# Performance work log

Hardware: AMD Instinct MI355X
Metric: run time of the kernel (lower is better)

The kernel has to match this reference:

```python
import jax, jax.numpy as jnp
import numpy as np

B, S, D, H = 4, 2048, 1024, 16
HD = D // H


def setup_inputs() -> dict:
    key = jax.random.key(0)
    ks = jax.random.split(key, 5)
    scale = 0.02
    return {
        "x": jax.random.normal(ks[0], (B, S, D), dtype=jnp.float32),
        "Wq": jax.random.normal(ks[1], (D, D), dtype=jnp.float32) * scale,
        "Wk": jax.random.normal(ks[2], (D, D), dtype=jnp.float32) * scale,
        "Wv": jax.random.normal(ks[3], (D, D), dtype=jnp.float32) * scale,
        "Wo": jax.random.normal(ks[4], (D, D), dtype=jnp.float32) * scale,
    }


def reference(x, Wq, Wk, Wv, Wo):
    b, s, d = x.shape
    # Linear layers (torch Linear: y = x @ W.T), no bias
    q = jnp.einsum('bsd,ed->bse', x, Wq).reshape(b, s, H, HD).transpose(0, 2, 1, 3)
    k = jnp.einsum('bsd,ed->bse', x, Wk).reshape(b, s, H, HD).transpose(0, 2, 1, 3)
    v = jnp.einsum('bsd,ed->bse', x, Wv).reshape(b, s, H, HD).transpose(0, 2, 1, 3)
    # [B,H,S,S] attention scores
    scores = jnp.einsum('bhqd,bhkd->bhqk', q, k)
    causal = jnp.tril(jnp.ones((s, s), dtype=bool))
    scores = jnp.where(causal, scores, -jnp.inf)
    # faithful to source: mask first, then scale, then softmax
    weights = jax.nn.softmax(scores / jnp.sqrt(jnp.float32(HD)), axis=-1)
    # dropout p=0.0 (eval): identity
    ctx = jnp.einsum('bhqk,bhkd->bhqd', weights, v)
    ctx = ctx.transpose(0, 2, 1, 3).reshape(b, s, d)
    return jnp.einsum('bsd,ed->bse', ctx, Wo)
```

## Files before the change

kernel.cpp:

```cpp
#include <hip/hip_runtime.h>
#include <math.h>

typedef unsigned short u16;
typedef __attribute__((ext_vector_type(8))) short short8;
typedef __attribute__((ext_vector_type(4))) float f32x4;
typedef __attribute__((ext_vector_type(16))) float f32x16;
typedef __attribute__((ext_vector_type(4))) unsigned int u32x4;

constexpr int Bb = 4, S_LEN = 2048, DMODEL = 1024, NH = 16;
constexpr int MTOT = Bb * S_LEN;

#define QSCALE 0.18033688011112042f

__device__ __forceinline__ u16 f2bf(float f) {
    union { float f; unsigned u; } v; v.f = f;
    unsigned r = v.u + 0x7FFFu + ((v.u >> 16) & 1u);
    return (u16)(r >> 16);
}

__device__ __forceinline__ float exp2_fast(float x) {
#if __has_builtin(__builtin_amdgcn_exp2f)
    return __builtin_amdgcn_exp2f(x);
#else
    float r; asm("v_exp_f32 %0, %1" : "=v"(r) : "v"(x)); return r;
#endif
}

__device__ __forceinline__ unsigned pk_bf16(float s0, float s1) {
    unsigned pk;
    asm("v_cvt_pk_bf16_f32 %0, %1, %2" : "=v"(pk) : "v"(s0), "v"(s1));
    return pk;
}

__device__ __forceinline__ void load_lds16(const void* g, void* l) {
    __builtin_amdgcn_global_load_lds(
        (const __attribute__((address_space(1))) unsigned int*)g,
        (__attribute__((address_space(3))) unsigned int*)l, 16, 0, 0);
}

__global__ __launch_bounds__(256)
void cvt_all(const float* __restrict__ x,
             const float* __restrict__ w0, const float* __restrict__ w1,
             const float* __restrict__ w2, const float* __restrict__ w3,
             u16* __restrict__ xb, u16* __restrict__ b0, u16* __restrict__ b1,
             u16* __restrict__ b2, u16* __restrict__ b3)
{
    int gid = blockIdx.x * 256 + threadIdx.x;
    constexpr int NXo = (MTOT * DMODEL) / 8;
    constexpr int NWo = (DMODEL * DMODEL) / 8;
    const float* s; u16* d; int o;
    float sc = 1.0f;
    if (gid < NXo) { s = x; d = xb; o = gid; }
    else {
        int t = gid - NXo;
        int w = t >> 17;
        o = t & (NWo - 1);
        s = (w == 0) ? w0 : (w == 1) ? w1 : (w == 2) ? w2 : w3;
        d = (w == 0) ? b0 : (w == 1) ? b1 : (w == 2) ? b2 : b3;
        if (w == 0) sc = QSCALE;
    }
    const float4* sp = (const float4*)(s + (size_t)o * 8);
    float4 a = sp[0], bq = sp[1];
    short8 ov;
    ov[0] = (short)f2bf(a.x * sc);  ov[1] = (short)f2bf(a.y * sc);
    ov[2] = (short)f2bf(a.z * sc);  ov[3] = (short)f2bf(a.w * sc);
    ov[4] = (short)f2bf(bq.x * sc); ov[5] = (short)f2bf(bq.y * sc);
    ov[6] = (short)f2bf(bq.z * sc); ov[7] = (short)f2bf(bq.w * sc);
    *(short8*)(d + (size_t)o * 8) = ov;
}

__global__ __launch_bounds__(256, 2)
void gemm_qkv(const u16* __restrict__ X,
              const u16* __restrict__ W0, const u16* __restrict__ W1, const u16* __restrict__ W2,
              u16* __restrict__ Qo, u16* __restrict__ Ko, u16* __restrict__ VT,
              int M, int N, int K)
{
    __shared__ __align__(16) u16 lds[3 * 128 * 64];
    u16* lA  = lds;
    u16* lB0 = lds + 128 * 64;
    u16* lB1 = lds + 2 * 128 * 64;

    const int tid  = threadIdx.x;
    const int wave = tid >> 6;
    const int lane = tid & 63;
    const int qd   = lane >> 4;
    const int c    = lane & 15;
    const int tm   = blockIdx.x * 128;
    const int tn   = blockIdx.y * 128;
    const int wm   = (wave >> 1) * 64;
    const int wn   = (wave & 1) * 64;

    if (blockIdx.z == 0) {
        f32x4 acc0[4][4] = {}, acc1[4][4] = {};

        for (int k0 = 0; k0 < K; k0 += 64) {
            if (k0) __syncthreads();
#pragma unroll
            for (int it = 0; it < 4; ++it) {
                int chunk = it * 256 + tid;
                int row = chunk >> 3, hc = chunk & 7;
                size_t ga = (size_t)(tm + row) * K + k0 + hc * 8;
                size_t gb = (size_t)(tn + row) * K + k0 + hc * 8;
                int ldo = (it * 256 + wave * 64) * 16;
                load_lds16(X  + ga, (char*)lA  + ldo);
                load_lds16(W0 + gb, (char*)lB0 + ldo);
                load_lds16(W1 + gb, (char*)lB1 + ldo);
            }
            __syncthreads();

#pragma unroll
            for (int kk = 0; kk < 64; kk += 32) {
                short8 a[4], b[4];
#pragma unroll
                for (int i = 0; i < 4; ++i)
                    a[i] = *(const short8*)&lA[(wm + i * 16 + c) * 64 + kk + qd * 8];
#pragma unroll
                for (int i = 0; i < 4; ++i)
                    b[i] = *(const short8*)&lB0[(wn + i * 16 + c) * 64 + kk + qd * 8];
#pragma unroll
                for (int mi = 0; mi < 4; ++mi)
#pragma unroll
                    for (int ni = 0; ni < 4; ++ni)
                        acc0[mi][ni] = __builtin_amdgcn_mfma_f32_16x16x32_bf16(
                            a[mi], b[ni], acc0[mi][ni], 0, 0, 0);
#pragma unroll
                for (int i = 0; i < 4; ++i)
                    b[i] = *(const short8*)&lB1[(wn + i * 16 + c) * 64 + kk + qd * 8];
#pragma unroll
                for (int mi = 0; mi < 4; ++mi)
#pragma unroll
                    for (int ni = 0; ni < 4; ++ni)
                        acc1[mi][ni] = __builtin_amdgcn_mfma_f32_16x16x32_bf16(
                            a[mi], b[ni], acc1[mi][ni], 0, 0, 0);
            }
        }

#pragma unroll
        for (int mi = 0; mi < 4; ++mi)
#pragma unroll
            for (int ni = 0; ni < 4; ++ni)
#pragma unroll
                for (int r = 0; r < 4; r += 2) {
                    int row = tm + wm + mi * 16 + qd * 4 + r;
                    int col = tn + wn + ni * 16 + c;
                    unsigned pq = pk_bf16(acc0[mi][ni][r], acc0[mi][ni][r + 1]);
                    Qo[(size_t)row * N + col]       = (u16)(pq & 0xffffu);
                    Qo[(size_t)(row + 1) * N + col] = (u16)(pq >> 16);
                    unsigned pk = pk_bf16(acc1[mi][ni][r], acc1[mi][ni][r + 1]);
                    Ko[(size_t)row * N + col]       = (u16)(pk & 0xffffu);
                    Ko[(size_t)(row + 1) * N + col] = (u16)(pk >> 16);
                }
    } else {
        f32x4 acc[4][4] = {};

        for (int k0 = 0; k0 < K; k0 += 64) {
            if (k0) __syncthreads();
#pragma unroll
            for (int it = 0; it < 4; ++it) {
                int chunk = it * 256 + tid;
                int row = chunk >> 3, hc = chunk & 7;
                load_lds16(X + (size_t)(tm + row) * K + k0 + hc * 8,
                           (char*)lA + (it * 256 + wave * 64) * 16);
                load_lds16(W2 + (size_t)(tn + row) * K + k0 + hc * 8,
                           (char*)lB0 + (it * 256 + wave * 64) * 16);
            }
            __syncthreads();

#pragma unroll
            for (int kk = 0; kk < 64; kk += 32) {
                short8 a[4], b[4];
#pragma unroll
                for (int i = 0; i < 4; ++i) {
                    a[i] = *(const short8*)&lA[(wm + i * 16 + c) * 64 + kk + qd * 8];
                    b[i] = *(const short8*)&lB0[(wn + i * 16 + c) * 64 + kk + qd * 8];
                }
#pragma unroll
                for (int mi = 0; mi < 4; ++mi)
#pragma unroll
                    for (int ni = 0; ni < 4; ++ni)
                        acc[mi][ni] = __builtin_amdgcn_mfma_f32_16x16x32_bf16(
                            a[mi], b[ni], acc[mi][ni], 0, 0, 0);
            }
        }

        __syncthreads();
        u16* Tw = lds + wave * 4096;
#pragma unroll
        for (int mi = 0; mi < 4; ++mi)
#pragma unroll
            for (int ni = 0; ni < 4; ++ni)
#pragma unroll
                for (int r = 0; r < 4; r += 2) {
                    unsigned pk = pk_bf16(acc[mi][ni][r], acc[mi][ni][r + 1]);
                    int r0 = mi * 16 + qd * 4 + r;
                    int cl = ni * 16 + c;
                    Tw[r0 * 64       + (cl ^ ((r0 << 1) & 0x38))]        = (u16)(pk & 0xffffu);
                    Tw[(r0 + 1) * 64 + (cl ^ (((r0 + 1) << 1) & 0x38))]  = (u16)(pk >> 16);
                }
        asm volatile("s_waitcnt lgkmcnt(0)" ::: "memory");

        const int b2   = tm >> 11;
        const int smb  = (tm & 2047) + wm;
        const int hgl  = (tn + wn) >> 6;
        const int sc8  = lane & 7;
#pragma unroll
        for (int it = 0; it < 8; ++it) {
            int hd = it * 8 + (lane >> 3);
            short8 o;
#pragma unroll
            for (int jj = 0; jj < 8; ++jj) {
                int rr = sc8 * 8 + jj;
                o[jj] = (short)Tw[rr * 64 + (hd ^ ((rr << 1) & 0x38))];
            }
            *(short8*)&VT[(size_t)((b2 * 16 + hgl) * 64 + hd) * S_LEN + smb + sc8 * 8] = o;
        }
    }
}

__global__ __launch_bounds__(256, 2)
void gemm_bt_f32(const u16* __restrict__ X, const u16* __restrict__ W,
                 float* __restrict__ Y, int M, int N, int K)
{
    __shared__ __align__(16) u16 lA[128 * 64];
    __shared__ __align__(16) u16 lB[128 * 64];

    const int tid  = threadIdx.x;
    const int wave = tid >> 6;
    const int lane = tid & 63;
    const int qd   = lane >> 4;
    const int c    = lane & 15;
    const int tm   = blockIdx.x * 128;
    const int tn   = blockIdx.y * 128;
    const int wm   = (wave >> 1) * 64;
    const int wn   = (wave & 1) * 64;

    f32x4 acc[4][4] = {};

    for (int k0 = 0; k0 < K; k0 += 64) {
        if (k0) __syncthreads();
#pragma unroll
        for (int it = 0; it < 4; ++it) {
            int chunk = it * 256 + tid;
            int row = chunk >> 3, hc = chunk & 7;
            load_lds16(X + (size_t)(tm + row) * K + k0 + hc * 8,
                       (char*)lA + (it * 256 + wave * 64) * 16);
            load_lds16(W + (size_t)(tn + row) * K + k0 + hc * 8,
                       (char*)lB + (it * 256 + wave * 64) * 16);
        }
        __syncthreads();

#pragma unroll
        for (int kk = 0; kk < 64; kk += 32) {
            short8 a[4], b[4];
#pragma unroll
            for (int i = 0; i < 4; ++i) {
                a[i] = *(const short8*)&lA[(wm + i * 16 + c) * 64 + kk + qd * 8];
                b[i] = *(const short8*)&lB[(wn + i * 16 + c) * 64 + kk + qd * 8];
            }
#pragma unroll
            for (int mi = 0; mi < 4; ++mi)
#pragma unroll
                for (int ni = 0; ni < 4; ++ni)
                    acc[mi][ni] = __builtin_amdgcn_mfma_f32_16x16x32_bf16(
                        a[mi], b[ni], acc[mi][ni], 0, 0, 0);
        }
    }

#pragma unroll
    for (int mi = 0; mi < 4; ++mi)
#pragma unroll
        for (int ni = 0; ni < 4; ++ni)
#pragma unroll
            for (int r = 0; r < 4; ++r) {
                int row = tm + wm + mi * 16 + qd * 4 + r;
                int col = tn + wn + ni * 16 + c;
                Y[(size_t)row * N + col] = acc[mi][ni][r];
            }
}

__global__ __launch_bounds__(512, 2)
void attention(const u16* __restrict__ Q, const u16* __restrict__ K,
               const u16* __restrict__ VT, u16* __restrict__ CTX)
{
    const int i  = blockIdx.x;
    const int j  = i & 255;
    const int bh = j >> 2;
    const int t  = j & 3;
    const int qt = (i >> 8) ? t : (7 - t);
    const int b = bh >> 4, h = bh & 15;

    __shared__ __align__(16) u16 lK[2][64 * 64];
    __shared__ __align__(16) u16 lV[2][64 * 64];

    const int tid = threadIdx.x, wave = tid >> 6, lane = tid & 63;
    const int l31 = lane & 31, hi = lane >> 5;
    const int wrow = wave * 32;
    const int srow = tid >> 3, shc = tid & 7;
    const int shcs = shc ^ (srow & 7);
    const int rxk  = l31 & 7;
    const size_t kbase = (size_t)(b * S_LEN) * DMODEL + h * 64;
    const size_t vbase = (size_t)(bh * 64) * S_LEN;

    const int q0 = qt * 256;
    const int nkv = 4 * qt + 4;
    const int qrg = q0 + wrow + l31;

    short8 qf[4];
#pragma unroll
    for (int ks = 0; ks < 4; ++ks)
        qf[ks] = *(const short8*)&Q[(size_t)(b * S_LEN + qrg) * DMODEL
                                    + h * 64 + ks * 16 + hi * 8];

    f32x16 oacc0 = {}, oacc1 = {};
    float psum = 0.f;

    load_lds16(K + kbase + (size_t)srow * DMODEL + shcs * 8,
               (char*)lK[0] + wave * 1024);
    load_lds16(VT + vbase + (size_t)srow * S_LEN + shcs * 8,
               (char*)lV[0] + wave * 1024);

    for (int kt = 0; kt < nkv; ++kt) {
        const int cur = kt & 1;
        const int k0 = kt * 64;

        __builtin_amdgcn_s_barrier();
        if (kt + 1 < nkv) {
            const int kn = (kt + 1) * 64;
            load_lds16(K + kbase + (size_t)(kn + srow) * DMODEL + shcs * 8,
                       (char*)lK[cur ^ 1] + wave * 1024);
            load_lds16(VT + vbase + (size_t)srow * S_LEN + kn + shcs * 8,
                       (char*)lV[cur ^ 1] + wave * 1024);
            asm volatile("s_waitcnt vmcnt(2)" ::: "memory");
        } else {
            asm volatile("s_waitcnt vmcnt(0)" ::: "memory");
        }
        __builtin_amdgcn_sched_barrier(0);
        __builtin_amdgcn_s_barrier();
        __builtin_amdgcn_sched_barrier(0);

        if (k0 <= q0 + wrow + 31) {
            f32x16 s0 = {}, s1 = {};
            __builtin_amdgcn_s_setprio(1);
#pragma unroll
            for (int hs = 0; hs < 4; ++hs) {
                const int sl = ((hs * 2 + hi) ^ rxk) << 3;
                short8 kf0 = *(const short8*)&lK[cur][l31 * 64 + sl];
                short8 kf1 = *(const short8*)&lK[cur][(32 + l31) * 64 + sl];
                s0 = __builtin_amdgcn_mfma_f32_32x32x16_bf16(kf0, qf[hs], s0, 0, 0, 0);
                s1 = __builtin_amdgcn_mfma_f32_32x32x16_bf16(kf1, qf[hs], s1, 0, 0, 0);
            }
            __builtin_amdgcn_s_setprio(0);

            float pva[16], pvb[16];
            if (k0 + 63 > q0 + wrow) {
                const int lim = qrg - k0 - 4 * hi;
#pragma unroll
                for (int r = 0; r < 16; ++r) {
                    const int ka = (r & 3) + 8 * (r >> 2);
                    pva[r] = (ka > lim)      ? -1.0e38f : s0[r];
                    pvb[r] = (ka + 32 > lim) ? -1.0e38f : s1[r];
                }
            } else {
#pragma unroll
                for (int r = 0; r < 16; ++r) { pva[r] = s0[r]; pvb[r] = s1[r]; }
            }
#pragma unroll
            for (int r = 0; r < 16; ++r) {
                pva[r] = exp2_fast(fminf(pva[r], 86.0f));
                pvb[r] = exp2_fast(fminf(pvb[r], 86.0f));
                psum += pva[r] + pvb[r];
            }
            unsigned own0[8], own1[8];
#pragma unroll
            for (int q = 0; q < 8; ++q) {
                own0[q] = pk_bf16(pva[2 * q], pva[2 * q + 1]);
                own1[q] = pk_bf16(pvb[2 * q], pvb[2 * q + 1]);
            }

            short8 paf[4];
#pragma unroll
            for (int f = 0; f < 4; ++f) {
                const unsigned* own = (f < 2) ? own0 : own1;
                const int base = (f & 1) * 4;
                unsigned a0 = own[base + 0], b0 = own[base + 2];
                unsigned a1 = own[base + 1], b1 = own[base + 3];
                asm("v_permlane32_swap_b32 %0, %1" : "+v"(a0), "+v"(b0));
                asm("v_permlane32_swap_b32 %0, %1" : "+v"(a1), "+v"(b1));
                u32x4 w; w[0] = a0; w[1] = a1; w[2] = b0; w[3] = b1;
                paf[f] = __builtin_bit_cast(short8, w);
            }

            __builtin_amdgcn_s_setprio(1);
#pragma unroll
            for (int ks = 0; ks < 4; ++ks) {
                const int vsl = ((ks * 2 + hi) ^ rxk) << 3;
                short8 vf0 = *(const short8*)&lV[cur][l31 * 64 + vsl];
                short8 vf1 = *(const short8*)&lV[cur][(32 + l31) * 64 + vsl];
                oacc0 = __builtin_amdgcn_mfma_f32_32x32x16_bf16(paf[ks], vf0, oacc0, 0, 0, 0);
                oacc1 = __builtin_amdgcn_mfma_f32_32x32x16_bf16(paf[ks], vf1, oacc1, 0, 0, 0);
            }
            __builtin_amdgcn_s_setprio(0);
        }
    }

    float pt = psum + __shfl_xor(psum, 32);
#pragma unroll
    for (int r = 0; r < 16; ++r) {
        const int orow = (r & 3) + 8 * (r >> 2) + 4 * hi;
        float inv = 1.0f / __shfl(pt, orow);
        const int rowg = q0 + wrow + orow;
        size_t base = (size_t)(b * S_LEN + rowg) * DMODEL + h * 64;
        unsigned pk = pk_bf16(oacc0[r] * inv, oacc1[r] * inv);
        CTX[base + l31]      = (u16)(pk & 0xffffu);
        CTX[base + 32 + l31] = (u16)(pk >> 16);
    }
}

extern "C" void kernel_launch(void* const* d_in, const int* in_sizes, int n_in,
                              void* d_out, int out_size, void* d_ws, size_t ws_size,
                              hipStream_t stream)
{
    const size_t MB = 1024 * 1024;
    char* ws = (char*)d_ws;
    if (ws_size < 72 * MB + 64) return;

    u16* xb  = (u16*)ws;
    u16* wb0 = (u16*)(ws + 16 * MB);
    u16* wb1 = (u16*)(ws + 18 * MB);
    u16* wb2 = (u16*)(ws + 20 * MB);
    u16* wb3 = (u16*)(ws + 22 * MB);
    u16* q   = (u16*)(ws + 24 * MB);
    u16* k   = (u16*)(ws + 40 * MB);
    u16* vt  = (u16*)(ws + 56 * MB);
    u16* ctx = xb;
    float* out = (float*)d_out;

    constexpr int NCVT = (MTOT * DMODEL + 4 * DMODEL * DMODEL) / 8 / 256;

    cvt_all<<<NCVT, 256, 0, stream>>>(
        (const float*)d_in[0], (const float*)d_in[1], (const float*)d_in[2],
        (const float*)d_in[3], (const float*)d_in[4], xb, wb0, wb1, wb2, wb3);

    gemm_qkv<<<dim3(MTOT / 128, DMODEL / 128, 2), 256, 0, stream>>>(
        xb, wb0, wb1, wb2, q, k, vt, MTOT, DMODEL, DMODEL);
    attention<<<512, 512, 0, stream>>>(q, k, vt, ctx);
    gemm_bt_f32<<<dim3(MTOT / 128, DMODEL / 128, 1), 256, 0, stream>>>(
        ctx, wb3, out, MTOT, DMODEL, DMODEL);
}
```

Measured before the change: 237.4 us.

## Software-pipeline attention so QK^T of the next tile overlaps softmax and PV

Restructures the attention KV loop so the QK^T MFMAs for tile kt are issued before the softmax and PV step for tile kt-1, carrying the previous scores in registers. V is triple-buffered in LDS so the previous tile's V stays valid while the next one is prefetched. The intent is to overlap exp/pack/permlane VALU work with matrix-core work across iterations. The cost is extra accumulator registers (two more f32x16), which could push spills or lower occupancy under launch_bounds(512,2), plus more LDS.

Result: slower. 249.2 us (+5.0%).

```diff
diff --git a/kernel.cpp b/kernel.cpp
--- a/kernel.cpp
+++ b/kernel.cpp
@@ -290,7 +290,7 @@
     const int b = bh >> 4, h = bh & 15;
 
     __shared__ __align__(16) u16 lK[2][64 * 64];
-    __shared__ __align__(16) u16 lV[2][64 * 64];
+    __shared__ __align__(16) u16 lV[3][64 * 64];
 
     const int tid = threadIdx.x, wave = tid >> 6, lane = tid & 63;
     const int l31 = lane & 31, hi = lane >> 5;
@@ -304,6 +304,7 @@
     const int q0 = qt * 256;
     const int nkv = 4 * qt + 4;
     const int qrg = q0 + wrow + l31;
+    const int wlim = q0 + wrow + 31;
 
     short8 qf[4];
 #pragma unroll
@@ -312,7 +313,58 @@
                                     + h * 64 + ks * 16 + hi * 8];
 
     f32x16 oacc0 = {}, oacc1 = {};
+    f32x16 sp0 = {}, sp1 = {};
     float psum = 0.f;
+
+    auto smpv = [&](const f32x16& s0v, const f32x16& s1v, int k0p, const u16* lVh) {
+        float pva[16], pvb[16];
+        if (k0p + 63 > q0 + wrow) {
+            const int lim = qrg - k0p - 4 * hi;
+#pragma unroll
+            for (int r = 0; r < 16; ++r) {
+                const int ka = (r & 3) + 8 * (r >> 2);
+                pva[r] = (ka > lim)      ? -1.0e38f : s0v[r];
+                pvb[r] = (ka + 32 > lim) ? -1.0e38f : s1v[r];
+            }
+        } else {
+#pragma unroll
+            for (int r = 0; r < 16; ++r) { pva[r] = s0v[r]; pvb[r] = s1v[r]; }
+        }
+#pragma unroll
+        for (int r = 0; r < 16; ++r) {
+            pva[r] = exp2_fast(fminf(pva[r], 86.0f));
+            pvb[r] = exp2_fast(fminf(pvb[r], 86.0f));
+            psum += pva[r] + pvb[r];
+        }
+        unsigned own0[8], own1[8];
+#pragma unroll
+        for (int q2 = 0; q2 < 8; ++q2) {
+            own0[q2] = pk_bf16(pva[2 * q2], pva[2 * q2 + 1]);
+            own1[q2] = pk_bf16(pvb[2 * q2], pvb[2 * q2 + 1]);
+        }
+        short8 paf[4];
+#pragma unroll
+        for (int f = 0; f < 4; ++f) {
+            const unsigned* own = (f < 2) ? own0 : own1;
+            const int base = (f & 1) * 4;
+            unsigned a0 = own[base + 0], b0 = own[base + 2];
+            unsigned a1 = own[base + 1], b1 = own[base + 3];
+            asm("v_permlane32_swap_b32 %0, %1" : "+v"(a0), "+v"(b0));
+            asm("v_permlane32_swap_b32 %0, %1" : "+v"(a1), "+v"(b1));
+            u32x4 w; w[0] = a0; w[1] = a1; w[2] = b0; w[3] = b1;
+            paf[f] = __builtin_bit_cast(short8, w);
+        }
+        __builtin_amdgcn_s_setprio(1);
+#pragma unroll
+        for (int ks = 0; ks < 4; ++ks) {
+            const int vsl = ((ks * 2 + hi) ^ rxk) << 3;
+            short8 vf0 = *(const short8*)&lVh[l31 * 64 + vsl];
+            short8 vf1 = *(const short8*)&lVh[(32 + l31) * 64 + vsl];
+            oacc0 = __builtin_amdgcn_mfma_f32_32x32x16_bf16(paf[ks], vf0, oacc0, 0, 0, 0);
+            oacc1 = __builtin_amdgcn_mfma_f32_32x32x16_bf16(paf[ks], vf1, oacc1, 0, 0, 0);
+        }
+        __builtin_amdgcn_s_setprio(0);
+    };
 
     load_lds16(K + kbase + (size_t)srow * DMODEL + shcs * 8,
                (char*)lK[0] + wave * 1024);
@@ -320,16 +372,13 @@
                (char*)lV[0] + wave * 1024);
 
     for (int kt = 0; kt < nkv; ++kt) {
-        const int cur = kt & 1;
-        const int k0 = kt * 64;
-
         __builtin_amdgcn_s_barrier();
         if (kt + 1 < nkv) {
             const int kn = (kt + 1) * 64;
             load_lds16(K + kbase + (size_t)(kn + srow) * DMODEL + shcs * 8,
-                       (char*)lK[cur ^ 1] + wave * 1024);
+                       (char*)lK[(kt + 1) & 1] + wave * 1024);
             load_lds16(VT + vbase + (size_t)srow * S_LEN + kn + shcs * 8,
-                       (char*)lV[cur ^ 1] + wave * 1024);
+                       (char*)lV[(kt + 1) % 3] + wave * 1024);
             asm volatile("s_waitcnt vmcnt(2)" ::: "memory");
         } else {
             asm volatile("s_waitcnt vmcnt(0)" ::: "memory");
@@ -338,69 +387,33 @@
         __builtin_amdgcn_s_barrier();
         __builtin_amdgcn_sched_barrier(0);
 
-        if (k0 <= q0 + wrow + 31) {
-            f32x16 s0 = {}, s1 = {};
+        const int k0 = kt * 64;
+
+        f32x16 sc0 = {}, sc1 = {};
+        if (k0 <= wlim) {
+            const u16* lKh = lK[kt & 1];
             __builtin_amdgcn_s_setprio(1);
 #pragma unroll
             for (int hs = 0; hs < 4; ++hs) {
                 const int sl = ((hs * 2 + hi) ^ rxk) << 3;
-                short8 kf0 = *(const short8*)&lK[cur][l31 * 64 + sl];
-                short8 kf1 = *(const short8*)&lK[cur][(32 + l31) * 64 + sl];
-                s0 = __builtin_amdgcn_mfma_f32_32x32x16_bf16(kf0, qf[hs], s0, 0, 0, 0);
-                s1 = __builtin_amdgcn_mfma_f32_32x32x16_bf16(kf1, qf[hs], s1, 0, 0, 0);
+                short8 kf0 = *(const short8*)&lKh[l31 * 64 + sl];
+                short8 kf1 = *(const short8*)&lKh[(32 + l31) * 64 + sl];
+                sc0 = __builtin_amdgcn_mfma_f32_32x32x16_bf16(kf0, qf[hs], sc0, 0, 0, 0);
+                sc1 = __builtin_amdgcn_mfma_f32_32x32x16_bf16(kf1, qf[hs], sc1, 0, 0, 0);
             }
             __builtin_amdgcn_s_setprio(0);
-
-            float pva[16], pvb[16];
-            if (k0 + 63 > q0 + wrow) {
-                const int lim = qrg - k0 - 4 * hi;
-#pragma unroll
-                for (int r = 0; r < 16; ++r) {
-                    const int ka = (r & 3) + 8 * (r >> 2);
-                    pva[r] = (ka > lim)      ? -1.0e38f : s0[r];
-                    pvb[r] = (ka + 32 > lim) ? -1.0e38f : s1[r];
-                }
-            } else {
-#pragma unroll
-                for (int r = 0; r < 16; ++r) { pva[r] = s0[r]; pvb[r] = s1[r]; }
-            }
-#pragma unroll
-            for (int r = 0; r < 16; ++r) {
-                pva[r] = exp2_fast(fminf(pva[r], 86.0f));
-                pvb[r] = exp2_fast(fminf(pvb[r], 86.0f));
-                psum += pva[r] + pvb[r];
-            }
-            unsigned own0[8], own1[8];
-#pragma unroll
-            for (int q = 0; q < 8; ++q) {
-                own0[q] = pk_bf16(pva[2 * q], pva[2 * q + 1]);
-                own1[q] = pk_bf16(pvb[2 * q], pvb[2 * q + 1]);
-            }
-
-            short8 paf[4];
-#pragma unroll
-            for (int f = 0; f < 4; ++f) {
-                const unsigned* own = (f < 2) ? own0 : own1;
-                const int base = (f & 1) * 4;
-                unsigned a0 = own[base + 0], b0 = own[base + 2];
-                unsigned a1 = own[base + 1], b1 = own[base + 3];
-                asm("v_permlane32_swap_b32 %0, %1" : "+v"(a0), "+v"(b0));
-                asm("v_permlane32_swap_b32 %0, %1" : "+v"(a1), "+v"(b1));
-                u32x4 w; w[0] = a0; w[1] = a1; w[2] = b0; w[3] = b1;
-                paf[f] = __builtin_bit_cast(short8, w);
-            }
-
-            __builtin_amdgcn_s_setprio(1);
-#pragma unroll
-            for (int ks = 0; ks < 4; ++ks) {
-                const int vsl = ((ks * 2 + hi) ^ rxk) << 3;
-                short8 vf0 = *(const short8*)&lV[cur][l31 * 64 + vsl];
-                short8 vf1 = *(const short8*)&lV[cur][(32 + l31) * 64 + vsl];
-                oacc0 = __builtin_amdgcn_mfma_f32_32x32x16_bf16(paf[ks], vf0, oacc0, 0, 0, 0);
-                oacc1 = __builtin_amdgcn_mfma_f32_32x32x16_bf16(paf[ks], vf1, oacc1, 0, 0, 0);
-            }
-            __builtin_amdgcn_s_setprio(0);
-        }
+        }
+
+        if (kt > 0 && (k0 - 64) <= wlim)
+            smpv(sp0, sp1, k0 - 64, &lV[(kt - 1) % 3][0]);
+
+        sp0 = sc0; sp1 = sc1;
+    }
+
+    {
+        const int k0p = (nkv - 1) * 64;
+        if (k0p <= wlim)
+            smpv(sp0, sp1, k0p, &lV[(nkv - 1) % 3][0]);
     }
 
     float pt = psum + __shfl_xor(psum, 32);
```
